# Kernel tuning notes

Measured on AMD Instinct MI355X. Metric: run time of the kernel, lower is better.

Reference implementation:

```python
import jax, jax.numpy as jnp
import numpy as np

N_NODES = 100000
N_EDGES = 1600000
F_IN = 128
EMB = 128
HEADS = 4
D_HEAD = EMB // HEADS
HIDDEN = 256
BATCH = 2048
CANDS = 16  # distractors + 1


def setup_inputs() -> dict:
    key = jax.random.key(0)
    ks = jax.random.split(key, 10)
    message = jax.random.normal(ks[0], (BATCH, HIDDEN), jnp.float32)
    x = jax.random.normal(ks[1], (N_NODES, F_IN), jnp.float32)
    edge_index = jax.random.randint(ks[2], (2, N_EDGES), 0, N_NODES, jnp.int64)
    indices = jax.random.randint(ks[3], (BATCH * CANDS,), 0, N_NODES, jnp.int64)
    s = 1.0 / np.sqrt(F_IN)
    W = jax.random.normal(ks[4], (F_IN, HEADS, D_HEAD), jnp.float32) * s
    att_src = jax.random.normal(ks[5], (HEADS, D_HEAD), jnp.float32) * s
    att_dst = jax.random.normal(ks[6], (HEADS, D_HEAD), jnp.float32) * s
    bias = jnp.zeros((EMB,), jnp.float32)
    fc_w = jax.random.normal(ks[7], (EMB, HIDDEN), jnp.float32) / np.sqrt(HIDDEN)
    fc_b = jnp.zeros((EMB,), jnp.float32)
    return {"message": message, "x": x, "edge_index": edge_index, "indices": indices,
            "W": W, "att_src": att_src, "att_dst": att_dst, "bias": bias,
            "fc_w": fc_w, "fc_b": fc_b}


def _gat(x, edge_index, W, att_src, att_dst, bias):
    N = x.shape[0]
    loops = jnp.arange(N, dtype=edge_index.dtype)
    src = jnp.concatenate([edge_index[0], loops])  # self-loops (PyG default)
    dst = jnp.concatenate([edge_index[1], loops])
    Wx = jnp.einsum('nf,fhd->nhd', x, W)                      # [N,H,D]
    a_s = (Wx * att_src).sum(-1)                              # [N,H]
    a_d = (Wx * att_dst).sum(-1)
    e = jax.nn.leaky_relu(a_s[src] + a_d[dst], 0.2)           # [E,H]
    m = jax.ops.segment_max(e, dst, num_segments=N)           # segment softmax
    ex = jnp.exp(e - m[dst])
    den = jax.ops.segment_sum(ex, dst, num_segments=N)
    alpha = ex / den[dst]
    out = jax.ops.segment_sum(alpha[:, :, None] * Wx[src], dst, num_segments=N)
    return out.reshape(N, -1) + bias                          # [N, H*D]


def reference(message, x, edge_index, indices, W, att_src, att_dst, bias, fc_w, fc_b):
    h = _gat(x, edge_index, W, att_src, att_dst, bias)        # [N, EMB]
    B = message.shape[0]
    emb = h[indices].reshape(B, -1, h.shape[-1])              # [B,C,EMB]
    msg = message @ fc_w.T + fc_b                             # [B,EMB]
    dots = jnp.einsum('bce,be->bc', emb, msg)                 # bmm scoring
    amax = jnp.abs(dots).max()
    tie = ((jnp.abs(dots) - amax) < 1e-10).astype(dots.dtype)
    noise = jax.random.normal(jax.random.key(42), dots.shape, dots.dtype)
    dots = dots + tie * amax * 1e-5 * noise
    return jax.nn.log_softmax(dots, axis=1)
```

## Files before the change

kernel.cpp:

```cpp
#include <hip/hip_runtime.h>
#include <stdint.h>
#include <stddef.h>

#define N_NODES 100000
#define N_EDGES 1600000
#define F_IN 128
#define EMB 128
#define HEADS 4
#define D_HEAD 32
#define HIDDEN 256
#define BATCH 2048
#define CANDS 16
#define NODE_B 391
#define MAXNEED 32768
#define WXBLOCKS 782
#define WTROWS 144
#define STR 136

typedef __attribute__((ext_vector_type(8))) short v8s;
typedef __attribute__((ext_vector_type(4))) float v4f;

__device__ __forceinline__ unsigned short f2bs(float f) {
  unsigned int u = __builtin_bit_cast(unsigned int, f);
  u = (u + 0x7fffu + ((u >> 16) & 1u)) >> 16;
  return (unsigned short)u;
}
__device__ __forceinline__ float bs2f(unsigned int s) {
  unsigned int u = (s & 0xffffu) << 16;
  return __builtin_bit_cast(float, u);
}

__global__ __launch_bounds__(256) void k_prep(const float* __restrict__ W,
                                              const float* __restrict__ att_src,
                                              const float* __restrict__ att_dst,
                                              unsigned short* __restrict__ Wtp,
                                              const int* __restrict__ idx,
                                              unsigned char* __restrict__ needed) {
  int i = blockIdx.x * 256 + threadIdx.x;
  if (i < 128 * STR) {
    int r = i / STR, c = i - r * STR;
    Wtp[i] = (c < 128) ? f2bs(W[c * 128 + r]) : (unsigned short)0;
  } else if (i < WTROWS * STR) {
    int ii = i - 128 * STR;
    int r = ii / STR, c = ii - r * STR;
    unsigned short v = 0;
    if (c < 128 && r < 8) {
      const float* att = (r < 4) ? att_src : att_dst;
      int hh = r & 3;
      float s = 0.f;
#pragma unroll
      for (int d = 0; d < 32; ++d) s += W[c * 128 + hh * 32 + d] * att[hh * 32 + d];
      v = f2bs(s);
    }
    Wtp[i] = v;
  }
  if (i < BATCH * CANDS) needed[idx[i]] = 1;
}

__global__ __launch_bounds__(256) void k_compact(const unsigned char* __restrict__ needed,
                                                 int* __restrict__ nidx,
                                                 int* __restrict__ nlist,
                                                 int* __restrict__ nw_cnt) {
  int i = blockIdx.x * 256 + threadIdx.x;
  if (i >= N_NODES) return;
  if (needed[i]) {
    int p = atomicAdd(nw_cnt, 1);
    nidx[i] = p + 1;
    nlist[p] = i;
  }
}

__global__ __launch_bounds__(256) void k_wx(const float* __restrict__ x,
                                            const unsigned short* __restrict__ Wtp,
                                            unsigned short* __restrict__ Wx,
                                            float* __restrict__ a_s,
                                            float* __restrict__ a_d) {
  __shared__ unsigned short wt[WTROWS * STR];
  __shared__ unsigned short xs[64 * STR];
  int tid = threadIdx.x;

  {
    const uint4* s = (const uint4*)Wtp;
    uint4* d = (uint4*)wt;
#pragma unroll
    for (int it = 0; it < 10; ++it) {
      int i = it * 256 + tid;
      if (i < WTROWS * STR / 8) d[i] = s[i];
    }
  }

  int w = tid >> 6, lane = tid & 63;
  int m = lane & 15, quad = lane >> 4;

  for (int chunk = 0; chunk < 2; ++chunk) {
    int rbase = blockIdx.x * 128 + chunk * 64;

    float4 f[8];
#pragma unroll
    for (int it = 0; it < 4; ++it) {
      int cid = it * 256 + tid;
      int row = cid >> 4, c = cid & 15;
      int gr = rbase + row;
      if (gr >= N_NODES) gr = N_NODES - 1;
      const float4* gp = (const float4*)(x + (size_t)gr * 128 + c * 8);
      f[2 * it] = gp[0];
      f[2 * it + 1] = gp[1];
    }
#pragma unroll
    for (int it = 0; it < 4; ++it) {
      int cid = it * 256 + tid;
      int row = cid >> 4, c = cid & 15;
      float4 f0 = f[2 * it], f1 = f[2 * it + 1];
      v8s a;
      a[0] = (short)f2bs(f0.x); a[1] = (short)f2bs(f0.y);
      a[2] = (short)f2bs(f0.z); a[3] = (short)f2bs(f0.w);
      a[4] = (short)f2bs(f1.x); a[5] = (short)f2bs(f1.y);
      a[6] = (short)f2bs(f1.z); a[7] = (short)f2bs(f1.w);
      *(v8s*)(&xs[row * STR + c * 8]) = a;
    }
    __syncthreads();

    v8s afrag[4];
#pragma unroll
    for (int t = 0; t < 4; ++t)
      afrag[t] = *(const v8s*)(&xs[(w * 16 + m) * STR + t * 32 + quad * 8]);

    v4f acc[9];
#pragma unroll
    for (int nt = 0; nt < 9; ++nt) {
      v4f a0 = {0.f, 0.f, 0.f, 0.f};
      const unsigned short* brow = wt + (size_t)(nt * 16 + m) * STR;
#pragma unroll
      for (int t = 0; t < 4; ++t) {
        v8s b = *(const v8s*)(brow + t * 32 + quad * 8);
        a0 = __builtin_amdgcn_mfma_f32_16x16x32_bf16(afrag[t], b, a0, 0, 0, 0);
      }
      acc[nt] = a0;
    }

#pragma unroll
    for (int r = 0; r < 4; ++r) {
      int orow = rbase + w * 16 + quad * 4 + r;
      if (orow < N_NODES) {
        if (m < 4) a_s[(size_t)orow * 4 + m] = acc[8][r];
        else if (m < 8) a_d[(size_t)orow * 4 + m - 4] = acc[8][r];
      }
    }

    __syncthreads();
#pragma unroll
    for (int nt = 0; nt < 8; ++nt)
#pragma unroll
      for (int r = 0; r < 4; ++r)
        xs[(w * 16 + quad * 4 + r) * STR + nt * 16 + m] = f2bs(acc[nt][r]);
    asm volatile("s_waitcnt lgkmcnt(0)" ::: "memory");
#pragma unroll
    for (int j = 0; j < 4; ++j) {
      int fr = 4 * j + (lane >> 4);
      int fc = (lane & 15) * 8;
      int grow = rbase + w * 16 + fr;
      v8s v = *(const v8s*)(&xs[(w * 16 + fr) * STR + fc]);
      if (grow < N_NODES) *(v8s*)(&Wx[(size_t)grow * 128 + fc]) = v;
    }
    __syncthreads();
  }
}

__global__ __launch_bounds__(256) void k_scatter(const int* __restrict__ ei,
                                                 const int* __restrict__ nidx,
                                                 int* __restrict__ cnt,
                                                 int* __restrict__ srclist) {
  int e = blockIdx.x * 256 + threadIdx.x;
  if (e >= N_EDGES) return;
  int dst = ei[N_EDGES + e];
  int ni = nidx[dst];
  if (!ni) return;
  ni--;
  int pos = atomicAdd(&cnt[ni], 1);
  if (pos < 64) srclist[ni * 64 + pos] = ei[e];
}

__global__ __launch_bounds__(256) void k_agg(const float* __restrict__ a_s,
                                             const float* __restrict__ a_d,
                                             const unsigned short* __restrict__ Wx,
                                             const int* __restrict__ nlist,
                                             const int* __restrict__ nw_cnt,
                                             const int* __restrict__ cnt,
                                             const int* __restrict__ srclist,
                                             const int* __restrict__ ei,
                                             const float* __restrict__ bias,
                                             unsigned short* __restrict__ hout) {
  __shared__ int sS[4][64];
  __shared__ float sW[4][256];
  int w = threadIdx.x >> 6, lane = threadIdx.x & 63;
  int wid = blockIdx.x * 4 + w;
  bool act = wid < nw_cnt[0];
  int dst = 0, degRaw = 0, deg = 0;
  float4 w4 = {0.f, 0.f, 0.f, 0.f};
  float4 ad4 = {0.f, 0.f, 0.f, 0.f};
  if (act) {
    dst = nlist[wid];
    degRaw = cnt[wid];
    deg = degRaw < 64 ? degRaw : 64;
    ad4 = *(const float4*)(a_d + (size_t)dst * 4);
    if (lane < deg) {
      int sv = srclist[wid * 64 + lane];
      float4 as = *(const float4*)(a_s + (size_t)sv * 4);
      float e0 = as.x + ad4.x; e0 = e0 > 0.f ? e0 : 0.2f * e0;
      float e1 = as.y + ad4.y; e1 = e1 > 0.f ? e1 : 0.2f * e1;
      float e2 = as.z + ad4.z; e2 = e2 > 0.f ? e2 : 0.2f * e2;
      float e3 = as.w + ad4.w; e3 = e3 > 0.f ? e3 : 0.2f * e3;
      w4.x = __expf(e0); w4.y = __expf(e1);
      w4.z = __expf(e2); w4.w = __expf(e3);
      sS[w][lane] = sv;
      *(float4*)(&sW[w][lane * 4]) = w4;
    }
  }
  __syncthreads();
  if (!act) return;

  float4 as4 = *(const float4*)(a_s + (size_t)dst * 4);
  float s0 = as4.x + ad4.x; s0 = s0 > 0.f ? s0 : 0.2f * s0;
  float s1 = as4.y + ad4.y; s1 = s1 > 0.f ? s1 : 0.2f * s1;
  float s2 = as4.z + ad4.z; s2 = s2 > 0.f ? s2 : 0.2f * s2;
  float s3 = as4.w + ad4.w; s3 = s3 > 0.f ? s3 : 0.2f * s3;
  float w0 = __expf(s0), w1 = __expf(s1), w2 = __expf(s2), w3 = __expf(s3);

  if (degRaw > 64) {
    int hh2 = lane >> 4;
    float adH = hh2 < 2 ? (hh2 == 0 ? ad4.x : ad4.y) : (hh2 == 2 ? ad4.z : ad4.w);
    float4 dv = {0.f, 0.f, 0.f, 0.f};
    for (int e = lane; e < N_EDGES; e += 64) {
      if (ei[N_EDGES + e] == dst) {
        int sv = ei[e];
        float4 as = *(const float4*)(a_s + (size_t)sv * 4);
        float e0 = as.x + ad4.x; e0 = e0 > 0.f ? e0 : 0.2f * e0;
        float e1 = as.y + ad4.y; e1 = e1 > 0.f ? e1 : 0.2f * e1;
        float e2 = as.z + ad4.z; e2 = e2 > 0.f ? e2 : 0.2f * e2;
        float e3 = as.w + ad4.w; e3 = e3 > 0.f ? e3 : 0.2f * e3;
        dv.x += __expf(e0); dv.y += __expf(e1);
        dv.z += __expf(e2); dv.w += __expf(e3);
      }
    }
#pragma unroll
    for (int o = 32; o >= 1; o >>= 1) {
      dv.x += __shfl_xor(dv.x, o); dv.y += __shfl_xor(dv.y, o);
      dv.z += __shfl_xor(dv.z, o); dv.w += __shfl_xor(dv.w, o);
    }
    float wSelfH = hh2 < 2 ? (hh2 == 0 ? w0 : w1) : (hh2 == 2 ? w2 : w3);
    float den = wSelfH + (hh2 < 2 ? (hh2 == 0 ? dv.x : dv.y)
                                  : (hh2 == 2 ? dv.z : dv.w));
    unsigned int us = *(const unsigned int*)(Wx + (size_t)dst * 128 + 2 * lane);
    float accP = wSelfH * bs2f(us), accQ = wSelfH * bs2f(us >> 16);
    for (int base = 0; base < N_EDGES; base += 64) {
      int e = base + lane;
      bool mm = (e < N_EDGES) && (ei[N_EDGES + e] == dst);
      unsigned long long mask = __ballot(mm);
      int svL = mm ? ei[e] : 0;
      while (mask) {
        int b = __ffsll(mask) - 1;
        mask &= mask - 1;
        int sv = __shfl(svL, b);
        float ash = a_s[(size_t)sv * 4 + hh2];
        float ee = ash + adH; ee = ee > 0.f ? ee : 0.2f * ee;
        float wA = __expf(ee);
        unsigned int u = *(const unsigned int*)(Wx + (size_t)sv * 128 + 2 * lane);
        accP += wA * bs2f(u); accQ += wA * bs2f(u >> 16);
      }
    }
    float inv = 1.0f / den;
    float2 b2 = *(const float2*)(bias + 2 * lane);
    unsigned int packed = (unsigned int)f2bs(accP * inv + b2.x)
                        | ((unsigned int)f2bs(accQ * inv + b2.y) << 16);
    *(unsigned int*)(hout + (size_t)dst * 128 + 2 * lane) = packed;
    return;
  }

  int half = lane >> 5, li = lane & 31, hh = li >> 3;

  float4 denv = w4;
#pragma unroll
  for (int o = 32; o >= 1; o >>= 1) {
    denv.x += __shfl_xor(denv.x, o);
    denv.y += __shfl_xor(denv.y, o);
    denv.z += __shfl_xor(denv.z, o);
    denv.w += __shfl_xor(denv.w, o);
  }
  float wSelf = hh < 2 ? (hh == 0 ? w0 : w1) : (hh == 2 ? w2 : w3);
  float denE = hh < 2 ? (hh == 0 ? denv.x : denv.y) : (hh == 2 ? denv.z : denv.w);
  float den = denE + wSelf;

  float acc0 = 0.f, acc1 = 0.f, acc2 = 0.f, acc3 = 0.f;
  if (half == 0) {
    uint2 u = *(const uint2*)(Wx + (size_t)dst * 128 + li * 4);
    acc0 = wSelf * bs2f(u.x); acc1 = wSelf * bs2f(u.x >> 16);
    acc2 = wSelf * bs2f(u.y); acc3 = wSelf * bs2f(u.y >> 16);
  }

  int j = 0;
#pragma unroll 4
  for (; j + 1 < deg; j += 2) {
    int jj = j + half;
    int s = sS[w][jj];
    float wA = sW[w][jj * 4 + hh];
    uint2 u = *(const uint2*)(Wx + (size_t)s * 128 + li * 4);
    acc0 += wA * bs2f(u.x); acc1 += wA * bs2f(u.x >> 16);
    acc2 += wA * bs2f(u.y); acc3 += wA * bs2f(u.y >> 16);
  }
  if (j < deg && half == 0) {
    int s = sS[w][j];
    float wA = sW[w][j * 4 + hh];
    uint2 u = *(const uint2*)(Wx + (size_t)s * 128 + li * 4);
    acc0 += wA * bs2f(u.x); acc1 += wA * bs2f(u.x >> 16);
    acc2 += wA * bs2f(u.y); acc3 += wA * bs2f(u.y >> 16);
  }

  acc0 += __shfl_xor(acc0, 32);
  acc1 += __shfl_xor(acc1, 32);
  acc2 += __shfl_xor(acc2, 32);
  acc3 += __shfl_xor(acc3, 32);

  if (half == 0) {
    float inv = 1.0f / den;
    float4 b4 = *(const float4*)(bias + li * 4);
    float r0 = acc0 * inv + b4.x;
    float r1 = acc1 * inv + b4.y;
    float r2 = acc2 * inv + b4.z;
    float r3 = acc3 * inv + b4.w;
    uint2 o;
    o.x = (unsigned int)f2bs(r0) | ((unsigned int)f2bs(r1) << 16);
    o.y = (unsigned int)f2bs(r2) | ((unsigned int)f2bs(r3) << 16);
    *(uint2*)(hout + (size_t)dst * 128 + li * 4) = o;
  }
}

__global__ __launch_bounds__(256) void k_msgscore(const float* __restrict__ message,
                                                  const float* __restrict__ fc_w,
                                                  const float* __restrict__ fc_b,
                                                  const unsigned short* __restrict__ h,
                                                  const int* __restrict__ indices,
                                                  float* __restrict__ out) {
  __shared__ float Sm[16][256];
  float* red = &Sm[0][0];
  int tid = threadIdx.x;
  int b0 = blockIdx.x * 16;
  for (int i = tid; i < 16 * 256; i += 256)
    Sm[i >> 8][i & 255] = message[(size_t)b0 * 256 + i];
  __syncthreads();
  int e = tid & 127, half = tid >> 7;
  float acc[16];
#pragma unroll
  for (int r = 0; r < 16; ++r) acc[r] = 0.f;
  const float* wrow = fc_w + (size_t)e * 256 + half * 128;
  for (int k = 0; k < 128; k += 4) {
    float4 w4 = *(const float4*)(wrow + k);
#pragma unroll
    for (int r = 0; r < 16; ++r) {
      float4 m4 = *(const float4*)(&Sm[r][half * 128 + k]);
      acc[r] += m4.x * w4.x + m4.y * w4.y + m4.z * w4.z + m4.w * w4.w;
    }
  }
  __syncthreads();
  if (half == 0) {
#pragma unroll
    for (int r = 0; r < 16; ++r) red[r * 128 + e] = acc[r];
  }
  __syncthreads();
  if (half == 1) {
#pragma unroll
    for (int r = 0; r < 16; ++r) red[r * 128 + e] += acc[r];
  }
  __syncthreads();
  for (int i = tid; i < 2048; i += 256) red[i] += fc_b[i & 127];
  __syncthreads();

  int r = tid >> 4, c = tid & 15;
  int idx = indices[(b0 + r) * 16 + c];
  const unsigned short* hr = h + (size_t)idx * 128;
  const float* mr = red + r * 128;
  float dot = 0.f;
#pragma unroll
  for (int k = 0; k < 128; k += 8) {
    uint4 q = *(const uint4*)(hr + k);
    float4 m0 = *(const float4*)(mr + k);
    float4 m1 = *(const float4*)(mr + k + 4);
    dot += bs2f(q.x) * m0.x + bs2f(q.x >> 16) * m0.y
         + bs2f(q.y) * m0.z + bs2f(q.y >> 16) * m0.w
         + bs2f(q.z) * m1.x + bs2f(q.z >> 16) * m1.y
         + bs2f(q.w) * m1.z + bs2f(q.w >> 16) * m1.w;
  }
  float mx = dot;
#pragma unroll
  for (int o = 1; o < 16; o <<= 1) mx = fmaxf(mx, __shfl_xor(mx, o));
  float ex = __expf(dot - mx);
  float sum = ex;
#pragma unroll
  for (int o = 1; o < 16; o <<= 1) sum += __shfl_xor(sum, o);
  float lse = mx + __logf(sum);
  out[(b0 + r) * 16 + c] = dot - lse;
}

extern "C" void kernel_launch(void* const* d_in, const int* in_sizes, int n_in,
                              void* d_out, int out_size, void* d_ws, size_t ws_size,
                              hipStream_t stream) {
  (void)in_sizes; (void)n_in; (void)out_size; (void)ws_size;
  const float* message = (const float*)d_in[0];
  const float* x       = (const float*)d_in[1];
  const int*   ei      = (const int*)d_in[2];
  const int*   indices = (const int*)d_in[3];
  const float* W       = (const float*)d_in[4];
  const float* att_src = (const float*)d_in[5];
  const float* att_dst = (const float*)d_in[6];
  const float* bias    = (const float*)d_in[7];
  const float* fc_w    = (const float*)d_in[8];
  const float* fc_b    = (const float*)d_in[9];
  float* out = (float*)d_out;

  char* p = (char*)d_ws;
  auto alloc = [&](size_t bytes) -> char* {
    char* r = p;
    p += (bytes + 255) & ~(size_t)255;
    return r;
  };
  unsigned short* Wx = (unsigned short*)alloc((size_t)N_NODES * 128 * 2);
  unsigned short* h  = (unsigned short*)alloc((size_t)N_NODES * 128 * 2);
  float* a_s = (float*)alloc((size_t)N_NODES * 4 * 4);
  float* a_d = (float*)alloc((size_t)N_NODES * 4 * 4);
  unsigned short* Wtp = (unsigned short*)alloc((size_t)WTROWS * STR * 2);
  unsigned char* needed = (unsigned char*)alloc((size_t)N_NODES);
  int* nidx      = (int*)alloc((size_t)N_NODES * 4);
  int* cnt       = (int*)alloc((size_t)MAXNEED * 4);
  int* nw_cnt    = (int*)alloc(4);
  int* nlist     = (int*)alloc((size_t)MAXNEED * 4);
  int* srclist   = (int*)alloc((size_t)MAXNEED * 64 * 4);

  hipMemsetAsync(needed, 0, (size_t)((char*)nlist - (char*)needed), stream);

  k_prep<<<128, 256, 0, stream>>>(W, att_src, att_dst, Wtp, indices, needed);
  k_compact<<<NODE_B, 256, 0, stream>>>(needed, nidx, nlist, nw_cnt);
  k_wx<<<WXBLOCKS, 256, 0, stream>>>(x, Wtp, Wx, a_s, a_d);
  k_scatter<<<N_EDGES / 256, 256, 0, stream>>>(ei, nidx, cnt, srclist);
  k_agg<<<MAXNEED / 4, 256, 0, stream>>>(a_s, a_d, Wx, nlist, nw_cnt, cnt, srclist, ei, bias, h);
  k_msgscore<<<BATCH / 16, 256, 0, stream>>>(message, fc_w, fc_b, h, indices, out);
}
```

Measured before the change: 212.2 us.

## Assign one node per 16-lane quarter-wave in aggregation and fuse compaction into prep

The aggregation kernel now handles four destination nodes per wavefront, 16 lanes each. Each lane loads 8 bf16 features with one uint4, and the denominator is reduced over 16 lanes, so about a quarter as many blocks are launched. The needed-node compaction moves into the prep kernel via an atomic first-touch mark, which removes one kernel launch and the full scan over all nodes. In exchange, the rare high-degree fallback becomes a serial per-lane scan over all edges, and per-lane work per edge grows.

```diff
diff --git a/kernel.cpp b/kernel.cpp
--- a/kernel.cpp
+++ b/kernel.cpp
@@ -11,7 +11,6 @@
 #define HIDDEN 256
 #define BATCH 2048
 #define CANDS 16
-#define NODE_B 391
 #define MAXNEED 32768
 #define WXBLOCKS 782
 #define WTROWS 144
@@ -35,7 +34,10 @@
                                               const float* __restrict__ att_dst,
                                               unsigned short* __restrict__ Wtp,
                                               const int* __restrict__ idx,
-                                              unsigned char* __restrict__ needed) {
+                                              int* __restrict__ mark,
+                                              int* __restrict__ nidx,
+                                              int* __restrict__ nlist,
+                                              int* __restrict__ nw_cnt) {
   int i = blockIdx.x * 256 + threadIdx.x;
   if (i < 128 * STR) {
     int r = i / STR, c = i - r * STR;
@@ -54,19 +56,13 @@
     }
     Wtp[i] = v;
   }
-  if (i < BATCH * CANDS) needed[idx[i]] = 1;
-}
-
-__global__ __launch_bounds__(256) void k_compact(const unsigned char* __restrict__ needed,
-                                                 int* __restrict__ nidx,
-                                                 int* __restrict__ nlist,
-                                                 int* __restrict__ nw_cnt) {
-  int i = blockIdx.x * 256 + threadIdx.x;
-  if (i >= N_NODES) return;
-  if (needed[i]) {
-    int p = atomicAdd(nw_cnt, 1);
-    nidx[i] = p + 1;
-    nlist[p] = i;
+  if (i < BATCH * CANDS) {
+    int v = idx[i];
+    if (atomicAdd(&mark[v], 1) == 0) {
+      int p = atomicAdd(nw_cnt, 1);
+      nidx[v] = p + 1;
+      nlist[p] = v;
+    }
   }
 }
 
@@ -190,148 +186,110 @@
                                              const int* __restrict__ ei,
                                              const float* __restrict__ bias,
                                              unsigned short* __restrict__ hout) {
-  __shared__ int sS[4][64];
-  __shared__ float sW[4][256];
+  __shared__ int sS[16][64];
+  __shared__ float sW[16][64 * 4];
   int w = threadIdx.x >> 6, lane = threadIdx.x & 63;
-  int wid = blockIdx.x * 4 + w;
+  int q = lane >> 4, li = lane & 15;
+  int wq = w * 4 + q;
+  int wid = (blockIdx.x * 4 + w) * 4 + q;
   bool act = wid < nw_cnt[0];
   int dst = 0, degRaw = 0, deg = 0;
-  float4 w4 = {0.f, 0.f, 0.f, 0.f};
   float4 ad4 = {0.f, 0.f, 0.f, 0.f};
+  float4 dsum = {0.f, 0.f, 0.f, 0.f};
   if (act) {
     dst = nlist[wid];
     degRaw = cnt[wid];
     deg = degRaw < 64 ? degRaw : 64;
     ad4 = *(const float4*)(a_d + (size_t)dst * 4);
-    if (lane < deg) {
-      int sv = srclist[wid * 64 + lane];
+    for (int t = li; t < deg; t += 16) {
+      int sv = srclist[wid * 64 + t];
       float4 as = *(const float4*)(a_s + (size_t)sv * 4);
       float e0 = as.x + ad4.x; e0 = e0 > 0.f ? e0 : 0.2f * e0;
       float e1 = as.y + ad4.y; e1 = e1 > 0.f ? e1 : 0.2f * e1;
       float e2 = as.z + ad4.z; e2 = e2 > 0.f ? e2 : 0.2f * e2;
       float e3 = as.w + ad4.w; e3 = e3 > 0.f ? e3 : 0.2f * e3;
+      float4 w4;
       w4.x = __expf(e0); w4.y = __expf(e1);
       w4.z = __expf(e2); w4.w = __expf(e3);
-      sS[w][lane] = sv;
-      *(float4*)(&sW[w][lane * 4]) = w4;
+      sS[wq][t] = sv;
+      *(float4*)(&sW[wq][t * 4]) = w4;
+      dsum.x += w4.x; dsum.y += w4.y; dsum.z += w4.z; dsum.w += w4.w;
     }
   }
   __syncthreads();
   if (!act) return;
 
+#pragma unroll
+  for (int o = 8; o >= 1; o >>= 1) {
+    dsum.x += __shfl_xor(dsum.x, o);
+    dsum.y += __shfl_xor(dsum.y, o);
+    dsum.z += __shfl_xor(dsum.z, o);
+    dsum.w += __shfl_xor(dsum.w, o);
+  }
+
+  int hh = li >> 2;
   float4 as4 = *(const float4*)(a_s + (size_t)dst * 4);
   float s0 = as4.x + ad4.x; s0 = s0 > 0.f ? s0 : 0.2f * s0;
   float s1 = as4.y + ad4.y; s1 = s1 > 0.f ? s1 : 0.2f * s1;
   float s2 = as4.z + ad4.z; s2 = s2 > 0.f ? s2 : 0.2f * s2;
   float s3 = as4.w + ad4.w; s3 = s3 > 0.f ? s3 : 0.2f * s3;
   float w0 = __expf(s0), w1 = __expf(s1), w2 = __expf(s2), w3 = __expf(s3);
+  float wSelf = hh < 2 ? (hh == 0 ? w0 : w1) : (hh == 2 ? w2 : w3);
+  float denE = hh < 2 ? (hh == 0 ? dsum.x : dsum.y) : (hh == 2 ? dsum.z : dsum.w);
+  float den = denE + wSelf;
+
+  float acc[8];
+  {
+    uint4 u = *(const uint4*)(Wx + (size_t)dst * 128 + li * 8);
+    acc[0] = wSelf * bs2f(u.x); acc[1] = wSelf * bs2f(u.x >> 16);
+    acc[2] = wSelf * bs2f(u.y); acc[3] = wSelf * bs2f(u.y >> 16);
+    acc[4] = wSelf * bs2f(u.z); acc[5] = wSelf * bs2f(u.z >> 16);
+    acc[6] = wSelf * bs2f(u.w); acc[7] = wSelf * bs2f(u.w >> 16);
+  }
 
   if (degRaw > 64) {
-    int hh2 = lane >> 4;
-    float adH = hh2 < 2 ? (hh2 == 0 ? ad4.x : ad4.y) : (hh2 == 2 ? ad4.z : ad4.w);
-    float4 dv = {0.f, 0.f, 0.f, 0.f};
-    for (int e = lane; e < N_EDGES; e += 64) {
+    float adH = hh < 2 ? (hh == 0 ? ad4.x : ad4.y) : (hh == 2 ? ad4.z : ad4.w);
+    den = wSelf;
+    for (int e = 0; e < N_EDGES; ++e) {
       if (ei[N_EDGES + e] == dst) {
         int sv = ei[e];
-        float4 as = *(const float4*)(a_s + (size_t)sv * 4);
-        float e0 = as.x + ad4.x; e0 = e0 > 0.f ? e0 : 0.2f * e0;
-        float e1 = as.y + ad4.y; e1 = e1 > 0.f ? e1 : 0.2f * e1;
-        float e2 = as.z + ad4.z; e2 = e2 > 0.f ? e2 : 0.2f * e2;
-        float e3 = as.w + ad4.w; e3 = e3 > 0.f ? e3 : 0.2f * e3;
-        dv.x += __expf(e0); dv.y += __expf(e1);
-        dv.z += __expf(e2); dv.w += __expf(e3);
-      }
-    }
-#pragma unroll
-    for (int o = 32; o >= 1; o >>= 1) {
-      dv.x += __shfl_xor(dv.x, o); dv.y += __shfl_xor(dv.y, o);
-      dv.z += __shfl_xor(dv.z, o); dv.w += __shfl_xor(dv.w, o);
-    }
-    float wSelfH = hh2 < 2 ? (hh2 == 0 ? w0 : w1) : (hh2 == 2 ? w2 : w3);
-    float den = wSelfH + (hh2 < 2 ? (hh2 == 0 ? dv.x : dv.y)
-                                  : (hh2 == 2 ? dv.z : dv.w));
-    unsigned int us = *(const unsigned int*)(Wx + (size_t)dst * 128 + 2 * lane);
-    float accP = wSelfH * bs2f(us), accQ = wSelfH * bs2f(us >> 16);
-    for (int base = 0; base < N_EDGES; base += 64) {
-      int e = base + lane;
-      bool mm = (e < N_EDGES) && (ei[N_EDGES + e] == dst);
-      unsigned long long mask = __ballot(mm);
-      int svL = mm ? ei[e] : 0;
-      while (mask) {
-        int b = __ffsll(mask) - 1;
-        mask &= mask - 1;
-        int sv = __shfl(svL, b);
-        float ash = a_s[(size_t)sv * 4 + hh2];
+        float ash = a_s[(size_t)sv * 4 + hh];
         float ee = ash + adH; ee = ee > 0.f ? ee : 0.2f * ee;
         float wA = __expf(ee);
-        unsigned int u = *(const unsigned int*)(Wx + (size_t)sv * 128 + 2 * lane);
-        accP += wA * bs2f(u); accQ += wA * bs2f(u >> 16);
+        den += wA;
+        uint4 u = *(const uint4*)(Wx + (size_t)sv * 128 + li * 8);
+        acc[0] += wA * bs2f(u.x); acc[1] += wA * bs2f(u.x >> 16);
+        acc[2] += wA * bs2f(u.y); acc[3] += wA * bs2f(u.y >> 16);
+        acc[4] += wA * bs2f(u.z); acc[5] += wA * bs2f(u.z >> 16);
+        acc[6] += wA * bs2f(u.w); acc[7] += wA * bs2f(u.w >> 16);
       }
     }
-    float inv = 1.0f / den;
-    float2 b2 = *(const float2*)(bias + 2 * lane);
-    unsigned int packed = (unsigned int)f2bs(accP * inv + b2.x)
-                        | ((unsigned int)f2bs(accQ * inv + b2.y) << 16);
-    *(unsigned int*)(hout + (size_t)dst * 128 + 2 * lane) = packed;
-    return;
-  }
-
-  int half = lane >> 5, li = lane & 31, hh = li >> 3;
-
-  float4 denv = w4;
-#pragma unroll
-  for (int o = 32; o >= 1; o >>= 1) {
-    denv.x += __shfl_xor(denv.x, o);
-    denv.y += __shfl_xor(denv.y, o);
-    denv.z += __shfl_xor(denv.z, o);
-    denv.w += __shfl_xor(denv.w, o);
-  }
-  float wSelf = hh < 2 ? (hh == 0 ? w0 : w1) : (hh == 2 ? w2 : w3);
-  float denE = hh < 2 ? (hh == 0 ? denv.x : denv.y) : (hh == 2 ? denv.z : denv.w);
-  float den = denE + wSelf;
-
-  float acc0 = 0.f, acc1 = 0.f, acc2 = 0.f, acc3 = 0.f;
-  if (half == 0) {
-    uint2 u = *(const uint2*)(Wx + (size_t)dst * 128 + li * 4);
-    acc0 = wSelf * bs2f(u.x); acc1 = wSelf * bs2f(u.x >> 16);
-    acc2 = wSelf * bs2f(u.y); acc3 = wSelf * bs2f(u.y >> 16);
-  }
-
-  int j = 0;
+  } else {
 #pragma unroll 4
-  for (; j + 1 < deg; j += 2) {
-    int jj = j + half;
-    int s = sS[w][jj];
-    float wA = sW[w][jj * 4 + hh];
-    uint2 u = *(const uint2*)(Wx + (size_t)s * 128 + li * 4);
-    acc0 += wA * bs2f(u.x); acc1 += wA * bs2f(u.x >> 16);
-    acc2 += wA * bs2f(u.y); acc3 += wA * bs2f(u.y >> 16);
-  }
-  if (j < deg && half == 0) {
-    int s = sS[w][j];
-    float wA = sW[w][j * 4 + hh];
-    uint2 u = *(const uint2*)(Wx + (size_t)s * 128 + li * 4);
-    acc0 += wA * bs2f(u.x); acc1 += wA * bs2f(u.x >> 16);
-    acc2 += wA * bs2f(u.y); acc3 += wA * bs2f(u.y >> 16);
-  }
-
-  acc0 += __shfl_xor(acc0, 32);
-  acc1 += __shfl_xor(acc1, 32);
-  acc2 += __shfl_xor(acc2, 32);
-  acc3 += __shfl_xor(acc3, 32);
-
-  if (half == 0) {
-    float inv = 1.0f / den;
-    float4 b4 = *(const float4*)(bias + li * 4);
-    float r0 = acc0 * inv + b4.x;
-    float r1 = acc1 * inv + b4.y;
-    float r2 = acc2 * inv + b4.z;
-    float r3 = acc3 * inv + b4.w;
-    uint2 o;
-    o.x = (unsigned int)f2bs(r0) | ((unsigned int)f2bs(r1) << 16);
-    o.y = (unsigned int)f2bs(r2) | ((unsigned int)f2bs(r3) << 16);
-    *(uint2*)(hout + (size_t)dst * 128 + li * 4) = o;
-  }
+    for (int j = 0; j < deg; ++j) {
+      int s = sS[wq][j];
+      float wA = sW[wq][j * 4 + hh];
+      uint4 u = *(const uint4*)(Wx + (size_t)s * 128 + li * 8);
+      acc[0] += wA * bs2f(u.x); acc[1] += wA * bs2f(u.x >> 16);
+      acc[2] += wA * bs2f(u.y); acc[3] += wA * bs2f(u.y >> 16);
+      acc[4] += wA * bs2f(u.z); acc[5] += wA * bs2f(u.z >> 16);
+      acc[6] += wA * bs2f(u.w); acc[7] += wA * bs2f(u.w >> 16);
+    }
+  }
+
+  float inv = 1.0f / den;
+  float4 b0 = *(const float4*)(bias + li * 8);
+  float4 b1 = *(const float4*)(bias + li * 8 + 4);
+  uint4 o;
+  o.x = (unsigned int)f2bs(acc[0] * inv + b0.x)
+      | ((unsigned int)f2bs(acc[1] * inv + b0.y) << 16);
+  o.y = (unsigned int)f2bs(acc[2] * inv + b0.z)
+      | ((unsigned int)f2bs(acc[3] * inv + b0.w) << 16);
+  o.z = (unsigned int)f2bs(acc[4] * inv + b1.x)
+      | ((unsigned int)f2bs(acc[5] * inv + b1.y) << 16);
+  o.w = (unsigned int)f2bs(acc[6] * inv + b1.z)
+      | ((unsigned int)f2bs(acc[7] * inv + b1.w) << 16);
+  *(uint4*)(hout + (size_t)dst * 128 + li * 8) = o;
 }
 
 __global__ __launch_bounds__(256) void k_msgscore(const float* __restrict__ message,
@@ -381,13 +339,13 @@
   float dot = 0.f;
 #pragma unroll
   for (int k = 0; k < 128; k += 8) {
-    uint4 q = *(const uint4*)(hr + k);
+    uint4 qv = *(const uint4*)(hr + k);
     float4 m0 = *(const float4*)(mr + k);
     float4 m1 = *(const float4*)(mr + k + 4);
-    dot += bs2f(q.x) * m0.x + bs2f(q.x >> 16) * m0.y
-         + bs2f(q.y) * m0.z + bs2f(q.y >> 16) * m0.w
-         + bs2f(q.z) * m1.x + bs2f(q.z >> 16) * m1.y
-         + bs2f(q.w) * m1.z + bs2f(q.w >> 16) * m1.w;
+    dot += bs2f(qv.x) * m0.x + bs2f(qv.x >> 16) * m0.y
+         + bs2f(qv.y) * m0.z + bs2f(qv.y >> 16) * m0.w
+         + bs2f(qv.z) * m1.x + bs2f(qv.z >> 16) * m1.y
+         + bs2f(qv.w) * m1.z + bs2f(qv.w >> 16) * m1.w;
   }
   float mx = dot;
 #pragma unroll
@@ -427,19 +385,18 @@
   float* a_s = (float*)alloc((size_t)N_NODES * 4 * 4);
   float* a_d = (float*)alloc((size_t)N_NODES * 4 * 4);
   unsigned short* Wtp = (unsigned short*)alloc((size_t)WTROWS * STR * 2);
-  unsigned char* needed = (unsigned char*)alloc((size_t)N_NODES);
+  int* mark      = (int*)alloc((size_t)N_NODES * 4);
   int* nidx      = (int*)alloc((size_t)N_NODES * 4);
   int* cnt       = (int*)alloc((size_t)MAXNEED * 4);
   int* nw_cnt    = (int*)alloc(4);
   int* nlist     = (int*)alloc((size_t)MAXNEED * 4);
   int* srclist   = (int*)alloc((size_t)MAXNEED * 64 * 4);
 
-  hipMemsetAsync(needed, 0, (size_t)((char*)nlist - (char*)needed), stream);
-
-  k_prep<<<128, 256, 0, stream>>>(W, att_src, att_dst, Wtp, indices, needed);
-  k_compact<<<NODE_B, 256, 0, stream>>>(needed, nidx, nlist, nw_cnt);
+  hipMemsetAsync(mark, 0, (size_t)((char*)nlist - (char*)mark), stream);
+
+  k_prep<<<128, 256, 0, stream>>>(W, att_src, att_dst, Wtp, indices, mark, nidx, nlist, nw_cnt);
   k_wx<<<WXBLOCKS, 256, 0, stream>>>(x, Wtp, Wx, a_s, a_d);
   k_scatter<<<N_EDGES / 256, 256, 0, stream>>>(ei, nidx, cnt, srclist);
-  k_agg<<<MAXNEED / 4, 256, 0, stream>>>(a_s, a_d, Wx, nlist, nw_cnt, cnt, srclist, ei, bias, h);
+  k_agg<<<MAXNEED / 16, 256, 0, stream>>>(a_s, a_d, Wx, nlist, nw_cnt, cnt, srclist, ei, bias, h);
   k_msgscore<<<BATCH / 16, 256, 0, stream>>>(message, fc_w, fc_b, h, indices, out);
 }
```

Result: faster. 194.1 us (-8.5%).
